# Optimization experiments

Hardware: AMD Instinct MI355X
Metric: run time of the kernel (lower is better)

## Reference

```python
import jax, jax.numpy as jnp
import numpy as np

NUM_HEADS = 4
KEY_DIM = 64
D_MODEL = 256
OUTPUT_DIM = 256


def setup_inputs() -> dict:
    key = jax.random.key(0)
    ks = jax.random.split(key, 11)
    B, T, D = 16, 1024, D_MODEL
    HD = NUM_HEADS * KEY_DIM
    s = 0.02
    return {
        "query": jax.random.normal(ks[0], (B, T, D), jnp.float32),
        "key": jax.random.normal(ks[1], (B, T, D), jnp.float32),
        "value": jax.random.normal(ks[2], (B, T, D), jnp.float32),
        "Wq": jax.random.normal(ks[3], (D, HD), jnp.float32) * s,
        "bq": jnp.zeros((HD,), jnp.float32),
        "Wk": jax.random.normal(ks[4], (D, HD), jnp.float32) * s,
        "bk": jnp.zeros((HD,), jnp.float32),
        "Wv": jax.random.normal(ks[5], (D, KEY_DIM), jnp.float32) * s,
        "bv": jnp.zeros((KEY_DIM,), jnp.float32),
        "Wo": jax.random.normal(ks[6], (HD, OUTPUT_DIM), jnp.float32) * s,
        "bo": jnp.zeros((OUTPUT_DIM,), jnp.float32),
    }


def reference(query, key, value, Wq, bq, Wk, bk, Wv, bv, Wo, bo):
    B, Tq, _ = query.shape
    Tk = key.shape[1]
    H, Dk = NUM_HEADS, KEY_DIM
    # projections
    q = (query @ Wq + bq).reshape(B, Tq, H, Dk)  # [B,Tq,H,Dk]
    k = (key @ Wk + bk).reshape(B, Tk, H, Dk)    # [B,Tk,H,Dk]
    v = value @ Wv + bv                           # [B,Tk,Dk] shared across heads
    scale = jnp.asarray(Dk, q.dtype) ** -0.5
    # scores [B,H,Tq,Tk]
    score = jnp.einsum("bqhd,bkhd->bhqk", q, k) * scale
    attn = jax.nn.softmax(score, axis=-1)
    # broadcast-V attention: [B,H,Tq,Tk] x [B,Tk,Dk] -> [B,H,Tq,Dk]
    out = jnp.einsum("bhqk,bkd->bhqd", attn, v)
    out = out.transpose(0, 2, 1, 3).reshape(B, Tq, H * Dk)
    return out @ Wo + bo
```

## Files before the change

### kernel.cpp

```cpp
#include <hip/hip_runtime.h>
#include <hip/hip_bf16.h>


typedef __attribute__((ext_vector_type(8))) short short8;
typedef __attribute__((ext_vector_type(4))) short s16x4;
typedef __attribute__((ext_vector_type(4))) float f32x4;

__device__ __forceinline__ short f2bf(float x) {
    return __builtin_bit_cast(short, __float2bfloat16(x));
}

__device__ __forceinline__ float exp2_fast(float x) {
#if __has_builtin(__builtin_amdgcn_exp2f)
    return __builtin_amdgcn_exp2f(x);
#else
    float r; asm("v_exp_f32 %0, %1" : "=v"(r) : "v"(x)); return r;
#endif
}

__device__ __forceinline__ f32x4 mfma16(short8 a, short8 b, f32x4 c) {
    return __builtin_amdgcn_mfma_f32_16x16x32_bf16(a, b, c, 0, 0, 0);
}
__device__ __forceinline__ f32x4 mfma16k16(s16x4 a, s16x4 b, f32x4 c) {
    return __builtin_amdgcn_mfma_f32_16x16x16bf16_1k(a, b, c, 0, 0, 0);
}

__device__ __forceinline__ void gll16(const float4* gsrc, float4* ldst) {
    __builtin_amdgcn_global_load_lds(
        (const __attribute__((address_space(1))) void*)gsrc,
        (__attribute__((address_space(3))) void*)ldst, 16, 0, 0);
}

#define QSCALE 0.18033688011112042f

__global__ void prep_weights(const float* __restrict__ Wq, const float* __restrict__ Wk,
                             const float* __restrict__ Wv, const float* __restrict__ Wo,
                             short* __restrict__ WqtF, short* __restrict__ WktF,
                             short* __restrict__ WvtF, short* __restrict__ WotF) {
    int tid = blockIdx.x * 256 + threadIdx.x;
    int k = tid >> 8, n = tid & 255;
    int off = ((n >> 6) << 14) + (((n >> 4) & 3) << 12) + ((k >> 5) << 9)
            + (((k >> 3) & 3) << 7) + ((n & 15) << 3) + (k & 7);
    WqtF[off] = f2bf(Wq[k * 256 + n] * QSCALE);
    WktF[off] = f2bf(Wk[k * 256 + n]);
    WotF[off] = f2bf(Wo[k * 256 + n]);
    if (n < 64) {
        int offv = ((n >> 4) << 12) + ((k >> 5) << 9) + (((k >> 3) & 3) << 7)
                 + ((n & 15) << 3) + (k & 7);
        WvtF[offv] = f2bf(Wv[k * 64 + n]);
    }
}

__global__ __launch_bounds__(256) void proj_all(
        const float* __restrict__ query, const float* __restrict__ key_,
        const float* __restrict__ value,
        const short* __restrict__ WqtF, const short* __restrict__ WktF,
        const short* __restrict__ WvtF,
        const float* __restrict__ bq, const float* __restrict__ bk,
        const float* __restrict__ bv,
        short* __restrict__ qf, short* __restrict__ kf, short* __restrict__ vf) {
    __shared__ short At[8192];
    const int tid = threadIdx.x;
    const int lane = tid & 63, wave = tid >> 6;
    const int u = lane >> 4, r16 = lane & 15;
    const int m0 = blockIdx.x * 32;
    const int task = blockIdx.y;

    const float* A = task == 0 ? query : (task == 1 ? key_ : value);

    #pragma unroll
    for (int j = 0; j < 4; ++j) {
        int p8 = j * 8 + ((wave >> 1) << 2) + u;
        int row = ((wave & 1) << 4) + r16;
        const float* src = A + (m0 + row) * 256 + p8 * 8;
        float4 a0 = *(const float4*)src;
        float4 a1 = *(const float4*)(src + 4);
        short8 w;
        w[0] = f2bf(a0.x); w[1] = f2bf(a0.y); w[2] = f2bf(a0.z); w[3] = f2bf(a0.w);
        w[4] = f2bf(a1.x); w[5] = f2bf(a1.y); w[6] = f2bf(a1.z); w[7] = f2bf(a1.w);
        int dst = ((p8 >> 2) << 10) + ((wave & 1) << 9) + ((p8 & 3) << 7) + (r16 << 3);
        *(short8*)&At[dst] = w;
    }

    const int b = m0 >> 10, t64 = (m0 & 1023) >> 6, half = (m0 >> 5) & 1;

    if (task < 2) {
        const short* WtF = task == 0 ? WqtF : WktF;
        const float* bias = task == 0 ? bq : bk;
        const float bscale = task == 0 ? QSCALE : 1.0f;
        short* outF = task == 0 ? qf : kf;
        const short* wb = WtF + (wave << 14);

        short8 bf8[4];
        #pragma unroll
        for (int g = 0; g < 4; ++g) bf8[g] = *(const short8*)&wb[(g << 12) + lane * 8];
        __syncthreads();

        f32x4 acc[2][4] = {};
        #pragma unroll
        for (int kk = 0; kk < 8; ++kk) {
            short8 af[2], nb[4];
            #pragma unroll
            for (int f = 0; f < 2; ++f) af[f] = *(const short8*)&At[(kk << 10) + (f << 9) + lane * 8];
            if (kk < 7) {
                #pragma unroll
                for (int g = 0; g < 4; ++g) nb[g] = *(const short8*)&wb[(g << 12) + ((kk + 1) << 9) + lane * 8];
            }
            #pragma unroll
            for (int f = 0; f < 2; ++f)
                #pragma unroll
                for (int g = 0; g < 4; ++g)
                    acc[f][g] = mfma16(af[f], bf8[g], acc[f][g]);
            #pragma unroll
            for (int g = 0; g < 4; ++g) bf8[g] = nb[g];
        }

        float bvv[4];
        #pragma unroll
        for (int g = 0; g < 4; ++g) bvv[g] = bias[(wave << 6) + 16 * g + r16] * bscale;
        short* ob = outF + ((((b << 2) + wave) << 4) + t64) * 4096;
        #pragma unroll
        for (int f = 0; f < 2; ++f) {
            int fg = half * 2 + f;
            #pragma unroll
            for (int g = 0; g < 4; ++g) {
                int base = (fg << 10) + ((g >> 1) << 9)
                         + (((2 * g + (r16 >> 3)) & 3) << 7) + (r16 & 7);
                #pragma unroll
                for (int rr = 0; rr < 4; ++rr)
                    ob[base + (4 * u + rr) * 8] = f2bf(acc[f][g][rr] + bvv[g]);
            }
        }
    } else {
        const int f = wave >> 1;
        short8 bf8[2];
        #pragma unroll
        for (int z = 0; z < 2; ++z) {
            int dg = ((wave & 1) << 1) + z;
            bf8[z] = *(const short8*)&WvtF[(dg << 12) + lane * 8];
        }
        __syncthreads();

        f32x4 acc[2] = {};
        #pragma unroll
        for (int kk = 0; kk < 8; ++kk) {
            short8 af = *(const short8*)&At[(kk << 10) + (f << 9) + lane * 8];
            short8 nb[2];
            if (kk < 7) {
                #pragma unroll
                for (int z = 0; z < 2; ++z) {
                    int dg = ((wave & 1) << 1) + z;
                    nb[z] = *(const short8*)&WvtF[(dg << 12) + ((kk + 1) << 9) + lane * 8];
                }
            }
            #pragma unroll
            for (int z = 0; z < 2; ++z) acc[z] = mfma16(af, bf8[z], acc[z]);
            bf8[0] = nb[0]; bf8[1] = nb[1];
        }

        short* ob = vf + ((b << 4) + t64) * 4096;
        const int gg = half * 2 + f;
        #pragma unroll
        for (int z = 0; z < 2; ++z) {
            int dg = ((wave & 1) << 1) + z;
            float bvv = bv[16 * dg + r16];
            s16x4 o;
            #pragma unroll
            for (int rr = 0; rr < 4; ++rr) o[rr] = f2bf(acc[z][rr] + bvv);
            *(s16x4*)&ob[(dg << 10) + ((gg >> 1) << 9) + lane * 8 + ((gg & 1) << 2)] = o;
        }
    }
}

__global__ __launch_bounds__(512, 2) void attn_og(const short* __restrict__ qF,
        const short* __restrict__ kF, const short* __restrict__ vF,
        const short* __restrict__ WoF, const float* __restrict__ bo,
        float* __restrict__ outp) {
    __shared__ float4 KV3[3840];
    const int tid = threadIdx.x;
    const int lane = tid & 63, wave = tid >> 6;
    const int u = lane >> 4, r16 = lane & 15;
    const int h = wave & 3, qh = wave >> 2;

    const int L = (blockIdx.x & 7) * 32 + (blockIdx.x >> 3);
    const int b = L >> 4, qt = L & 15;

    const short* qb = qF + (((b << 2) + h) << 16) + (qt << 12);
    short8 qfr[2][2];
    #pragma unroll
    for (int f = 0; f < 2; ++f)
        #pragma unroll
        for (int c = 0; c < 2; ++c)
            qfr[f][c] = *(const short8*)&qb[((2 * qh + f) << 10) + (c << 9) + lane * 8];

    #define STAGE(t, bufp)                                                          \
        {                                                                           \
            _Pragma("unroll")                                                       \
            for (int j_ = 0; j_ < 3; ++j_) {                                        \
                int ch_ = wave + 8 * j_;                                            \
                if (ch_ < 20) {                                                     \
                    const float4* src_;                                             \
                    if (ch_ < 16)                                                   \
                        src_ = (const float4*)kF + (((b << 2) + (ch_ >> 2)) * 8192) \
                             + (t) * 256 + ((ch_ & 3) << 6) + lane;                 \
                    else                                                            \
                        src_ = (const float4*)vF + (b * 8192) + ((t) >> 1) * 512    \
                             + ((ch_ - 16) << 7) + (((t) & 1) << 6) + lane;         \
                    gll16(src_, (bufp) + (ch_ << 6));                               \
                }                                                                   \
            }                                                                       \
        }

    float4* bc = KV3;
    float4* bn = KV3 + 1280;
    float4* bs = KV3 + 2560;

    STAGE(0, bc)
    STAGE(1, bn)
    asm volatile("s_waitcnt vmcnt(0)" ::: "memory");
    __builtin_amdgcn_s_barrier();

    f32x4 acc[2][4] = {};
    f32x4 accl[2] = {};
    s16x4 ones;
    { short o = (short)0x3F80; ones[0] = o; ones[1] = o; ones[2] = o; ones[3] = o; }

    for (int kt = 0; kt < 32; ++kt) {
        if (kt < 30) STAGE(kt + 2, bs)

        const short* Kh = (const short*)bc + (h << 11);
        const short* Vb = (const short*)bc + 8192;

        short8 kf8[4];
        #pragma unroll
        for (int g = 0; g < 2; ++g)
            #pragma unroll
            for (int c = 0; c < 2; ++c)
                kf8[g * 2 + c] = *(const short8*)&Kh[(g << 10) + (c << 9) + lane * 8];

        f32x4 s[2][2];
        __builtin_amdgcn_s_setprio(1);
        #pragma unroll
        for (int f = 0; f < 2; ++f)
            #pragma unroll
            for (int g = 0; g < 2; ++g) {
                f32x4 z = {};
                z = mfma16(kf8[2 * g], qfr[f][0], z);
                s[f][g] = mfma16(kf8[2 * g + 1], qfr[f][1], z);
            }
        __builtin_amdgcn_s_setprio(0);

        s16x4 pk[2][2];
        #pragma unroll
        for (int f = 0; f < 2; ++f)
            #pragma unroll
            for (int g = 0; g < 2; ++g)
                #pragma unroll
                for (int rr = 0; rr < 4; ++rr)
                    pk[f][g][rr] = f2bf(exp2_fast(s[f][g][rr]));

        __builtin_amdgcn_s_setprio(1);
        #pragma unroll
        for (int f = 0; f < 2; ++f)
            #pragma unroll
            for (int g = 0; g < 2; ++g)
                accl[f] = mfma16k16(ones, pk[f][g], accl[f]);
        #pragma unroll
        for (int dg = 0; dg < 4; ++dg) {
            short8 v8 = *(const short8*)&Vb[(dg << 9) + lane * 8];
            s16x4 vlo = { v8[0], v8[1], v8[2], v8[3] };
            s16x4 vhi = { v8[4], v8[5], v8[6], v8[7] };
            #pragma unroll
            for (int f = 0; f < 2; ++f) {
                acc[f][dg] = mfma16k16(vlo, pk[f][0], acc[f][dg]);
                acc[f][dg] = mfma16k16(vhi, pk[f][1], acc[f][dg]);
            }
        }
        __builtin_amdgcn_s_setprio(0);

        if (kt < 30) {
            if (wave < 4) asm volatile("s_waitcnt vmcnt(3)" ::: "memory");
            else          asm volatile("s_waitcnt vmcnt(2)" ::: "memory");
            __builtin_amdgcn_s_barrier();
        } else if (kt == 30) {
            asm volatile("s_waitcnt vmcnt(0)" ::: "memory");
            __builtin_amdgcn_s_barrier();
        }
        float4* t_ = bc; bc = bn; bn = bs; bs = t_;
    }
    #undef STAGE

    __syncthreads();

    short* At = (short*)KV3;
    float linv[2] = { 1.0f / accl[0][0], 1.0f / accl[1][0] };
    #pragma unroll
    for (int f = 0; f < 2; ++f)
        #pragma unroll
        for (int dg = 0; dg < 4; ++dg) {
            s16x4 o;
            #pragma unroll
            for (int rr = 0; rr < 4; ++rr) o[rr] = f2bf(acc[f][dg][rr] * linv[f]);
            int kk = 2 * h + (dg >> 1);
            int fq = 2 * qh + f;
            int u2 = 2 * (dg & 1) + (u >> 1);
            int off = (kk << 11) + (fq << 9) + ((u2 << 4) + r16) * 8 + ((u & 1) << 2);
            *(s16x4*)&At[off] = o;
        }
    __syncthreads();

    const short* wb = WoF + ((wave >> 1) << 14) + ((wave & 1) << 13);
    f32x4 acc2[4][2] = {};
    #pragma unroll
    for (int kk = 0; kk < 8; ++kk) {
        short8 af[4], bf2[2];
        #pragma unroll
        for (int fq = 0; fq < 4; ++fq) af[fq] = *(const short8*)&At[(kk << 11) + (fq << 9) + lane * 8];
        #pragma unroll
        for (int gg = 0; gg < 2; ++gg) bf2[gg] = *(const short8*)&wb[(gg << 12) + (kk << 9) + lane * 8];
        #pragma unroll
        for (int fq = 0; fq < 4; ++fq)
            #pragma unroll
            for (int gg = 0; gg < 2; ++gg)
                acc2[fq][gg] = mfma16(af[fq], bf2[gg], acc2[fq][gg]);
    }

    const int m0 = L << 6;
    float bvv[2];
    #pragma unroll
    for (int gg = 0; gg < 2; ++gg) bvv[gg] = bo[(wave << 5) + (gg << 4) + r16];
    #pragma unroll
    for (int fq = 0; fq < 4; ++fq)
        #pragma unroll
        for (int gg = 0; gg < 2; ++gg)
            #pragma unroll
            for (int rr = 0; rr < 4; ++rr)
                outp[(m0 + 16 * fq + 4 * u + rr) * 256 + (wave << 5) + (gg << 4) + r16]
                    = acc2[fq][gg][rr] + bvv[gg];
}

extern "C" void kernel_launch(void* const* d_in, const int* in_sizes, int n_in,
                              void* d_out, int out_size, void* d_ws, size_t ws_size,
                              hipStream_t stream) {
    (void)in_sizes; (void)n_in; (void)out_size; (void)ws_size;
    const float* query = (const float*)d_in[0];
    const float* key_  = (const float*)d_in[1];
    const float* value = (const float*)d_in[2];
    const float* Wq = (const float*)d_in[3];
    const float* bq = (const float*)d_in[4];
    const float* Wk = (const float*)d_in[5];
    const float* bk = (const float*)d_in[6];
    const float* Wv = (const float*)d_in[7];
    const float* bv = (const float*)d_in[8];
    const float* Wo = (const float*)d_in[9];
    const float* bo = (const float*)d_in[10];
    float* outp = (float*)d_out;

    short* wsp  = (short*)d_ws;
    short* WqtF = wsp;
    short* WktF = wsp + 65536;
    short* WotF = wsp + 131072;
    short* WvtF = wsp + 196608;
    short* qf   = wsp + 212992;
    short* kf   = wsp + 4407296;
    short* vf   = wsp + 8601600;

    hipLaunchKernelGGL(prep_weights, dim3(256), dim3(256), 0, stream,
                       Wq, Wk, Wv, Wo, WqtF, WktF, WvtF, WotF);
    hipLaunchKernelGGL(proj_all, dim3(512, 3), dim3(256), 0, stream,
                       query, key_, value, WqtF, WktF, WvtF, bq, bk, bv, qf, kf, vf);
    hipLaunchKernelGGL(attn_og, dim3(256), dim3(512), 0, stream,
                       qf, kf, vf, WotF, bo, outp);
}
```

Baseline: 61.88 us.

## Halve attention query tile to 32 rows and double grid to 512 blocks

Each attention block now handles 32 query rows instead of 64, with each wave owning one 16-row fragment instead of two. The grid doubles to 512 blocks and launch bounds ask for 4 blocks per CU, so more blocks run at once and fill all CUs (256 blocks under-filled the 256-CU device at 2 waves/SIMD). The cost is that each K/V tile is loaded from global memory and staged in LDS twice as often per query row, and each block does less MFMA work per staged tile. Register pressure drops, and the output-projection epilogue shrinks to match.

```diff
diff --git a/kernel.cpp b/kernel.cpp
--- a/kernel.cpp
+++ b/kernel.cpp
@@ -172,7 +172,7 @@
     }
 }
 
-__global__ __launch_bounds__(512, 2) void attn_og(const short* __restrict__ qF,
+__global__ __launch_bounds__(512, 4) void attn_og(const short* __restrict__ qF,
         const short* __restrict__ kF, const short* __restrict__ vF,
         const short* __restrict__ WoF, const float* __restrict__ bo,
         float* __restrict__ outp) {
@@ -182,16 +182,15 @@
     const int u = lane >> 4, r16 = lane & 15;
     const int h = wave & 3, qh = wave >> 2;
 
-    const int L = (blockIdx.x & 7) * 32 + (blockIdx.x >> 3);
-    const int b = L >> 4, qt = L & 15;
-
-    const short* qb = qF + (((b << 2) + h) << 16) + (qt << 12);
-    short8 qfr[2][2];
-    #pragma unroll
-    for (int f = 0; f < 2; ++f)
-        #pragma unroll
-        for (int c = 0; c < 2; ++c)
-            qfr[f][c] = *(const short8*)&qb[((2 * qh + f) << 10) + (c << 9) + lane * 8];
+    const int L = (blockIdx.x & 7) * 64 + (blockIdx.x >> 3);
+    const int b = L >> 5, qt = L & 31;
+
+    const short* qb = qF + (((b << 2) + h) << 16) + ((qt >> 1) << 12);
+    const int f64 = ((qt & 1) << 1) + qh;
+    short8 qfr[2];
+    #pragma unroll
+    for (int c = 0; c < 2; ++c)
+        qfr[c] = *(const short8*)&qb[(f64 << 10) + (c << 9) + lane * 8];
 
     #define STAGE(t, bufp)                                                          \
         {                                                                           \
@@ -220,8 +219,8 @@
     asm volatile("s_waitcnt vmcnt(0)" ::: "memory");
     __builtin_amdgcn_s_barrier();
 
-    f32x4 acc[2][4] = {};
-    f32x4 accl[2] = {};
+    f32x4 acc[4] = {};
+    f32x4 accl = {};
     s16x4 ones;
     { short o = (short)0x3F80; ones[0] = o; ones[1] = o; ones[2] = o; ones[3] = o; }
 
@@ -238,43 +237,33 @@
             for (int c = 0; c < 2; ++c)
                 kf8[g * 2 + c] = *(const short8*)&Kh[(g << 10) + (c << 9) + lane * 8];
 
-        f32x4 s[2][2];
+        f32x4 s[2];
         __builtin_amdgcn_s_setprio(1);
         #pragma unroll
-        for (int f = 0; f < 2; ++f)
-            #pragma unroll
-            for (int g = 0; g < 2; ++g) {
-                f32x4 z = {};
-                z = mfma16(kf8[2 * g], qfr[f][0], z);
-                s[f][g] = mfma16(kf8[2 * g + 1], qfr[f][1], z);
-            }
+        for (int g = 0; g < 2; ++g) {
+            f32x4 z = {};
+            z = mfma16(kf8[2 * g], qfr[0], z);
+            s[g] = mfma16(kf8[2 * g + 1], qfr[1], z);
+        }
         __builtin_amdgcn_s_setprio(0);
 
-        s16x4 pk[2][2];
-        #pragma unroll
-        for (int f = 0; f < 2; ++f)
-            #pragma unroll
-            for (int g = 0; g < 2; ++g)
-                #pragma unroll
-                for (int rr = 0; rr < 4; ++rr)
-                    pk[f][g][rr] = f2bf(exp2_fast(s[f][g][rr]));
+        s16x4 pk[2];
+        #pragma unroll
+        for (int g = 0; g < 2; ++g)
+            #pragma unroll
+            for (int rr = 0; rr < 4; ++rr)
+                pk[g][rr] = f2bf(exp2_fast(s[g][rr]));
 
         __builtin_amdgcn_s_setprio(1);
-        #pragma unroll
-        for (int f = 0; f < 2; ++f)
-            #pragma unroll
-            for (int g = 0; g < 2; ++g)
-                accl[f] = mfma16k16(ones, pk[f][g], accl[f]);
+        accl = mfma16k16(ones, pk[0], accl);
+        accl = mfma16k16(ones, pk[1], accl);
         #pragma unroll
         for (int dg = 0; dg < 4; ++dg) {
             short8 v8 = *(const short8*)&Vb[(dg << 9) + lane * 8];
             s16x4 vlo = { v8[0], v8[1], v8[2], v8[3] };
             s16x4 vhi = { v8[4], v8[5], v8[6], v8[7] };
-            #pragma unroll
-            for (int f = 0; f < 2; ++f) {
-                acc[f][dg] = mfma16k16(vlo, pk[f][0], acc[f][dg]);
-                acc[f][dg] = mfma16k16(vhi, pk[f][1], acc[f][dg]);
-            }
+            acc[dg] = mfma16k16(vlo, pk[0], acc[dg]);
+            acc[dg] = mfma16k16(vhi, pk[1], acc[dg]);
         }
         __builtin_amdgcn_s_setprio(0);
 
@@ -293,44 +282,41 @@
     __syncthreads();
 
     short* At = (short*)KV3;
-    float linv[2] = { 1.0f / accl[0][0], 1.0f / accl[1][0] };
-    #pragma unroll
-    for (int f = 0; f < 2; ++f)
-        #pragma unroll
-        for (int dg = 0; dg < 4; ++dg) {
-            s16x4 o;
-            #pragma unroll
-            for (int rr = 0; rr < 4; ++rr) o[rr] = f2bf(acc[f][dg][rr] * linv[f]);
-            int kk = 2 * h + (dg >> 1);
-            int fq = 2 * qh + f;
-            int u2 = 2 * (dg & 1) + (u >> 1);
-            int off = (kk << 11) + (fq << 9) + ((u2 << 4) + r16) * 8 + ((u & 1) << 2);
-            *(s16x4*)&At[off] = o;
-        }
+    float linv = 1.0f / accl[0];
+    #pragma unroll
+    for (int dg = 0; dg < 4; ++dg) {
+        s16x4 o;
+        #pragma unroll
+        for (int rr = 0; rr < 4; ++rr) o[rr] = f2bf(acc[dg][rr] * linv);
+        int kk = 2 * h + (dg >> 1);
+        int u2 = 2 * (dg & 1) + (u >> 1);
+        int off = (kk << 10) + (qh << 9) + (u2 << 7) + (r16 << 3) + ((u & 1) << 2);
+        *(s16x4*)&At[off] = o;
+    }
     __syncthreads();
 
     const short* wb = WoF + ((wave >> 1) << 14) + ((wave & 1) << 13);
-    f32x4 acc2[4][2] = {};
+    f32x4 acc2[2][2] = {};
     #pragma unroll
     for (int kk = 0; kk < 8; ++kk) {
-        short8 af[4], bf2[2];
-        #pragma unroll
-        for (int fq = 0; fq < 4; ++fq) af[fq] = *(const short8*)&At[(kk << 11) + (fq << 9) + lane * 8];
+        short8 af[2], bf2[2];
+        #pragma unroll
+        for (int fq = 0; fq < 2; ++fq) af[fq] = *(const short8*)&At[(kk << 10) + (fq << 9) + lane * 8];
         #pragma unroll
         for (int gg = 0; gg < 2; ++gg) bf2[gg] = *(const short8*)&wb[(gg << 12) + (kk << 9) + lane * 8];
         #pragma unroll
-        for (int fq = 0; fq < 4; ++fq)
+        for (int fq = 0; fq < 2; ++fq)
             #pragma unroll
             for (int gg = 0; gg < 2; ++gg)
                 acc2[fq][gg] = mfma16(af[fq], bf2[gg], acc2[fq][gg]);
     }
 
-    const int m0 = L << 6;
+    const int m0 = L << 5;
     float bvv[2];
     #pragma unroll
     for (int gg = 0; gg < 2; ++gg) bvv[gg] = bo[(wave << 5) + (gg << 4) + r16];
     #pragma unroll
-    for (int fq = 0; fq < 4; ++fq)
+    for (int fq = 0; fq < 2; ++fq)
         #pragma unroll
         for (int gg = 0; gg < 2; ++gg)
             #pragma unroll
@@ -369,6 +355,6 @@
                        Wq, Wk, Wv, Wo, WqtF, WktF, WvtF, WotF);
     hipLaunchKernelGGL(proj_all, dim3(512, 3), dim3(256), 0, stream,
                        query, key_, value, WqtF, WktF, WvtF, bq, bk, bv, qf, kf, vf);
-    hipLaunchKernelGGL(attn_og, dim3(256), dim3(512), 0, stream,
+    hipLaunchKernelGGL(attn_og, dim3(512), dim3(512), 0, stream,
                        qf, kf, vf, WotF, bo, outp);
 }
```

After: 60.73 us. About the same (-1.9%).
